# Kernel tuning notes

Measured on AMD Instinct MI355X. Metric: run time of the kernel, lower is better.

## Reference

```python
import jax, jax.numpy as jnp
import numpy as np

DIM = 512
HEADS = 8
DIM_HEAD = 64
SCALE = DIM_HEAD ** -0.5


def setup_inputs() -> dict:
    key = jax.random.key(0)
    k1, k2, k3, k4, k5 = jax.random.split(key, 5)
    inner = HEADS * DIM_HEAD
    x = jax.random.normal(k1, (16, DIM, 32, 32), dtype=jnp.float32)
    W_proj = jax.random.normal(k2, (DIM, inner * 3), dtype=jnp.float32) * (DIM ** -0.5)
    b_proj = jax.random.normal(k3, (inner * 3,), dtype=jnp.float32) * 0.01
    W_out = jax.random.normal(k4, (inner, DIM), dtype=jnp.float32) * (inner ** -0.5)
    b_out = jax.random.normal(k5, (DIM,), dtype=jnp.float32) * 0.01
    return {"x": x, "W_proj": W_proj, "b_proj": b_proj, "W_out": W_out, "b_out": b_out}


def reference(x, W_proj, b_proj, W_out, b_out):
    b, c, hh, ww = x.shape
    s = hh * ww
    xs = x.reshape(b, c, s).transpose(0, 2, 1)  # b s c
    qkv = xs @ W_proj + b_proj                  # b s (heads * 3*dim_head)
    qkv = qkv.reshape(b, s, HEADS, 3 * DIM_HEAD)
    q, k, v = jnp.split(qkv, 3, axis=-1)        # each: b s h d
    w = jnp.einsum('bshd,bthd->bsth', q, k) * SCALE
    w = jax.nn.softmax(w, axis=2)
    res = jnp.einsum('bsth,bthd->bshd', w, v).reshape(b, s, HEADS * DIM_HEAD)
    out = res @ W_out + b_out + xs              # b s c (residual)
    return out.transpose(0, 2, 1).reshape(b, c, hh, ww)
```

## Files before the change

kernel.cpp:

```cpp
#include <hip/hip_runtime.h>
#include <hip/hip_bf16.h>

#define BATCH 16
#define CDIM  512
#define SEQ   1024
#define HEADS 8
#define DHEAD 64
#define N3    1536
#define QSCALE 0.18033688011112042f

typedef unsigned short ushort_t;
typedef __attribute__((ext_vector_type(8))) short short8;
typedef __attribute__((ext_vector_type(4))) float f32x4;

__device__ __forceinline__ unsigned f2bf(float f) {
    unsigned u = __float_as_uint(f);
    u += 0x7fffu + ((u >> 16) & 1u);
    return u >> 16;
}
__device__ __forceinline__ float fast_exp2(float x) {
    float r;
    asm("v_exp_f32 %0, %1" : "=v"(r) : "v"(x));
    return r;
}
__device__ __forceinline__ unsigned pack_bf16_trunc(float lo, float hi) {
    return __builtin_amdgcn_perm(__float_as_uint(hi), __float_as_uint(lo), 0x07060302u);
}
__device__ __forceinline__ void async16(const void* g, void* l) {
    __builtin_amdgcn_global_load_lds(
        (const __attribute__((address_space(1))) unsigned int*)g,
        (__attribute__((address_space(3))) unsigned int*)l, 16, 0, 0);
}
__device__ __forceinline__ void barrier_raw() {
    __builtin_amdgcn_sched_barrier(0);
    __builtin_amdgcn_s_barrier();
    __builtin_amdgcn_sched_barrier(0);
}
#define WAIT_VMCNT(n) asm volatile("s_waitcnt vmcnt(" #n ")" ::: "memory")


__global__ __launch_bounds__(256) void blockify_kernel(
    const float* __restrict__ in, ushort_t* __restrict__ out, int C)
{
    __shared__ float t[64][65];
    const int k0 = blockIdx.y * 64, c0 = blockIdx.x * 64;
    const float* inb = in + (size_t)blockIdx.z * 512 * C;
    const int tid = threadIdx.x;
#pragma unroll
    for (int i = 0; i < 16; ++i) {
        int idx = tid + i * 256;
        int r = idx >> 6, c = idx & 63;
        t[r][c] = inb[(size_t)(k0 + r) * C + c0 + c];
    }
    __syncthreads();
    const size_t mbase = (size_t)blockIdx.z * C + c0;
    const int ml = tid & 63;
#pragma unroll
    for (int i = 0; i < 2; ++i) {
        int oct = (tid >> 6) + i * 4;
        size_t m = mbase + ml;
        int mt = (int)(m >> 7), mr = (int)(m & 127);
        int m16 = mr >> 4, col = mr & 15;
        int k = k0 + oct * 8;
        int it = k >> 5, q = (k >> 3) & 3;
        uint4 pk;
        pk.x = f2bf(t[oct * 8 + 0][ml]) | (f2bf(t[oct * 8 + 1][ml]) << 16);
        pk.y = f2bf(t[oct * 8 + 2][ml]) | (f2bf(t[oct * 8 + 3][ml]) << 16);
        pk.z = f2bf(t[oct * 8 + 4][ml]) | (f2bf(t[oct * 8 + 5][ml]) << 16);
        pk.w = f2bf(t[oct * 8 + 6][ml]) | (f2bf(t[oct * 8 + 7][ml]) << 16);
        size_t off = ((size_t)(mt * 16 + it) * 8 + m16) * 512 + (q * 16 + col) * 8;
        *(uint4*)&out[off] = pk;
    }
}

__global__ __launch_bounds__(256) void qkv_gemm_kernel(
    const ushort_t* __restrict__ xtb, const ushort_t* __restrict__ WpTb,
    const float* __restrict__ bp,
    ushort_t* __restrict__ q_buf, ushort_t* __restrict__ kb,
    ushort_t* __restrict__ vb)
{
    __shared__ alignas(16) ushort_t Asub[2][8 * 512];
    __shared__ alignas(16) ushort_t Bsub[2][8 * 512];

    const int tid = threadIdx.x, w = tid >> 6, lane = tid & 63;
    const int quad = lane >> 4, col = lane & 15;
    const int wm = w >> 1, wn = w & 1;

    const int lin = blockIdx.x + 12 * blockIdx.y;
    const int xcd = lin & 7;
    const int rr  = lin >> 3;
    const int n0  = (rr % 12) * 128;
    const int m0  = ((rr / 12) * 8 + xcd) * 128;

    f32x4 acc[4][4];
#pragma unroll
    for (int i = 0; i < 4; ++i)
#pragma unroll
        for (int j = 0; j < 4; ++j) acc[i][j] = (f32x4){0.f, 0.f, 0.f, 0.f};

    const ushort_t* Ab = xtb  + (size_t)(m0 >> 7) * 65536 + (w * 2) * 512 + lane * 8;
    const ushort_t* Bb = WpTb + (size_t)(n0 >> 7) * 65536 + (w * 2) * 512 + lane * 8;

#define QKV_STAGE(buf, t)                                         \
    do {                                                          \
        async16(Ab + (t) * 4096,       &Asub[buf][(w * 2 + 0) * 512]); \
        async16(Ab + (t) * 4096 + 512, &Asub[buf][(w * 2 + 1) * 512]); \
        async16(Bb + (t) * 4096,       &Bsub[buf][(w * 2 + 0) * 512]); \
        async16(Bb + (t) * 4096 + 512, &Bsub[buf][(w * 2 + 1) * 512]); \
    } while (0)

    QKV_STAGE(0, 0);
    QKV_STAGE(1, 1);
    for (int it = 0; it < 16; ++it) {
        const int cur = it & 1;
        if (it < 15) { WAIT_VMCNT(4); } else { WAIT_VMCNT(0); }
        barrier_raw();

        short8 af[4], bfr[4];
#pragma unroll
        for (int i = 0; i < 4; ++i) af[i]  = *(const short8*)&Asub[cur][(wm * 4 + i) * 512 + lane * 8];
#pragma unroll
        for (int j = 0; j < 4; ++j) bfr[j] = *(const short8*)&Bsub[cur][(wn * 4 + j) * 512 + lane * 8];
#pragma unroll
        for (int i = 0; i < 4; ++i)
#pragma unroll
            for (int j = 0; j < 4; ++j)
                acc[i][j] = __builtin_amdgcn_mfma_f32_16x16x32_bf16(af[i], bfr[j], acc[i][j], 0, 0, 0);

        if (it < 14) {
            barrier_raw();
            QKV_STAGE(cur, it + 2);
        }
    }
#undef QKV_STAGE

    const int b = m0 >> 10, s0 = m0 & 1023;
    const size_t b8 = (size_t)b * HEADS;
#pragma unroll
    for (int j = 0; j < 4; ++j) {
        int nb = n0 + wn * 64 + j * 16;
        int h = nb / 192, rem = nb % 192;
        int type = rem >> 6, dbase = rem & 63;
        float bias = bp[nb + col];
        size_t bh = b8 + h;
        int d = dbase + col;
#pragma unroll
        for (int i = 0; i < 4; ++i) {
            int sb = s0 + wm * 64 + i * 16 + quad * 4;
            f32x4 v = acc[i][j];
            if (type == 2) {
                unsigned lo = f2bf(v[0] + bias) | (f2bf(v[1] + bias) << 16);
                unsigned hi = f2bf(v[2] + bias) | (f2bf(v[3] + bias) << 16);
                uint2 pk; pk.x = lo; pk.y = hi;
                int itv = sb >> 6, sub = (d >> 4) * 2 + ((sb >> 5) & 1);
                size_t off = ((bh * 16 + itv) * 8 + sub) * 512
                           + (((sb >> 3) & 3) * 16 + (d & 15)) * 8 + (sb & 7);
                *(uint2*)&vb[off] = pk;
            } else if (type == 1) {
#pragma unroll
                for (int r = 0; r < 4; ++r) {
                    int t = sb + r;
                    int itk = t >> 6, sub = ((t >> 4) & 3) * 2 + (d >> 5);
                    size_t off = ((bh * 16 + itk) * 8 + sub) * 512
                               + (((d >> 3) & 3) * 16 + (t & 15)) * 8 + (d & 7);
                    kb[off] = (ushort_t)f2bf(v[r] + bias);
                }
            } else {
#pragma unroll
                for (int r = 0; r < 4; ++r)
                    q_buf[(bh * SEQ + sb + r) * DHEAD + d] =
                        (ushort_t)f2bf((v[r] + bias) * QSCALE);
            }
        }
    }
}

__global__ __launch_bounds__(128) void attn_kernel(
    const ushort_t* __restrict__ q_buf, const ushort_t* __restrict__ kb,
    const ushort_t* __restrict__ vb, ushort_t* __restrict__ resb)
{
    __shared__ alignas(16) ushort_t Kf[2][8 * 512];
    __shared__ alignas(16) ushort_t Vf[2][8 * 512];
    __shared__ alignas(16) ushort_t Pf[2 * 1024];

    const int tid  = threadIdx.x;
    const int w    = tid >> 6;
    const int lane = tid & 63;
    const int quad = lane >> 4;
    const int col  = lane & 15;

    const int bhid = blockIdx.x;
    const int b = bhid >> 3, h = bhid & 7;
    const int q0 = blockIdx.y * 128;
    const size_t bh = (size_t)b * HEADS + h;

    const ushort_t* qp = q_buf + ((bh * SEQ) + q0 + w * 64 + col) * DHEAD + quad * 8;
    short8 qf0[4], qf1[4];
#pragma unroll
    for (int g = 0; g < 4; ++g) {
        qf0[g] = *(const short8*)(qp + g * 16 * DHEAD);
        qf1[g] = *(const short8*)(qp + g * 16 * DHEAD + 32);
    }

    short8 ones;
#pragma unroll
    for (int i = 0; i < 8; ++i) ones[i] = (short)0x3F80;

    f32x4 O[4][4];
#pragma unroll
    for (int g = 0; g < 4; ++g)
#pragma unroll
        for (int i = 0; i < 4; ++i) O[g][i] = (f32x4){0.f, 0.f, 0.f, 0.f};
    f32x4 L[4];
#pragma unroll
    for (int g = 0; g < 4; ++g) L[g] = (f32x4){0.f, 0.f, 0.f, 0.f};

    const ushort_t* kaB = kb + (size_t)bh * 65536 + (w * 4) * 512 + lane * 8;
    const ushort_t* vaB = vb + (size_t)bh * 65536 + (w * 4) * 512 + lane * 8;

    const int poff_base = col * 8 + (quad & 1) * 4;
    const int qh = quad >> 1;
    ushort_t* pg = &Pf[w * 1024];

#define ATTN_STAGE(buf, t)                                          \
    do {                                                            \
        const ushort_t* ka_ = kaB + (size_t)(t) * 4096;             \
        const ushort_t* va_ = vaB + (size_t)(t) * 4096;             \
        async16(ka_,        &Kf[buf][(w * 4 + 0) * 512]);           \
        async16(ka_ + 512,  &Kf[buf][(w * 4 + 1) * 512]);           \
        async16(ka_ + 1024, &Kf[buf][(w * 4 + 2) * 512]);           \
        async16(ka_ + 1536, &Kf[buf][(w * 4 + 3) * 512]);           \
        async16(va_,        &Vf[buf][(w * 4 + 0) * 512]);           \
        async16(va_ + 512,  &Vf[buf][(w * 4 + 1) * 512]);           \
        async16(va_ + 1024, &Vf[buf][(w * 4 + 2) * 512]);           \
        async16(va_ + 1536, &Vf[buf][(w * 4 + 3) * 512]);           \
    } while (0)

    ATTN_STAGE(0, 0);
    ATTN_STAGE(1, 1);

    for (int it = 0; it < 16; ++it) {
        const int cur = it & 1;
        const ushort_t* kc = Kf[cur];
        const ushort_t* vc = Vf[cur];
        if (it < 15) { WAIT_VMCNT(8); } else { WAIT_VMCNT(0); }
        barrier_raw();

        short8 kf[8];
#pragma unroll
        for (int t16 = 0; t16 < 4; ++t16) {
            kf[2 * t16 + 0] = *(const short8*)&kc[(t16 * 2 + 0) * 512 + lane * 8];
            kf[2 * t16 + 1] = *(const short8*)&kc[(t16 * 2 + 1) * 512 + lane * 8];
        }

        short8 pf[4][2];
#pragma unroll
        for (int g = 0; g < 4; ++g) {
            f32x4 S[4];
            __builtin_amdgcn_s_setprio(1);
#pragma unroll
            for (int t16 = 0; t16 < 4; ++t16) {
                f32x4 a = (f32x4){0.f, 0.f, 0.f, 0.f};
                a = __builtin_amdgcn_mfma_f32_16x16x32_bf16(kf[2 * t16 + 0], qf0[g], a, 0, 0, 0);
                a = __builtin_amdgcn_mfma_f32_16x16x32_bf16(kf[2 * t16 + 1], qf1[g], a, 0, 0, 0);
                S[t16] = a;
            }
            __builtin_amdgcn_s_setprio(0);
#pragma unroll
            for (int t16 = 0; t16 < 4; ++t16) {
                uint2 pk;
                pk.x = pack_bf16_trunc(fast_exp2(S[t16][0]), fast_exp2(S[t16][1]));
                pk.y = pack_bf16_trunc(fast_exp2(S[t16][2]), fast_exp2(S[t16][3]));
                int off = (t16 >> 1) * 512 + (((t16 * 2) + qh) & 3) * 128 + poff_base;
                *(uint2*)&pg[off] = pk;
            }
            pf[g][0] = *(const short8*)&pg[lane * 8];
            pf[g][1] = *(const short8*)&pg[512 + lane * 8];
        }

#pragma unroll
        for (int d16 = 0; d16 < 4; ++d16) {
            const short8 v0 = *(const short8*)&vc[(d16 * 2 + 0) * 512 + lane * 8];
            const short8 v1 = *(const short8*)&vc[(d16 * 2 + 1) * 512 + lane * 8];
            __builtin_amdgcn_s_setprio(1);
#pragma unroll
            for (int g = 0; g < 4; ++g) {
                O[g][d16] = __builtin_amdgcn_mfma_f32_16x16x32_bf16(pf[g][0], v0, O[g][d16], 0, 0, 0);
                O[g][d16] = __builtin_amdgcn_mfma_f32_16x16x32_bf16(pf[g][1], v1, O[g][d16], 0, 0, 0);
            }
            __builtin_amdgcn_s_setprio(0);
        }
#pragma unroll
        for (int g = 0; g < 4; ++g) {
            L[g] = __builtin_amdgcn_mfma_f32_16x16x32_bf16(pf[g][0], ones, L[g], 0, 0, 0);
            L[g] = __builtin_amdgcn_mfma_f32_16x16x32_bf16(pf[g][1], ones, L[g], 0, 0, 0);
        }

        if (it < 14) {
            barrier_raw();
            ATTN_STAGE(cur, it + 2);
        }
    }
#undef ATTN_STAGE

    const int mt = b * 8 + (q0 >> 7);
#pragma unroll
    for (int g = 0; g < 4; ++g) {
        const int m16 = w * 4 + g;
#pragma unroll
        for (int r = 0; r < 4; ++r) {
            float inv = 1.f / L[g][r];
            const int mcol = quad * 4 + r;
#pragma unroll
            for (int d16 = 0; d16 < 4; ++d16) {
                int itk = h * 2 + (d16 >> 1);
                int kq = (d16 & 1) * 2 + (col >> 3);
                size_t off = ((size_t)(mt * 16 + itk) * 8 + m16) * 512
                           + (kq * 16 + mcol) * 8 + (col & 7);
                resb[off] = (ushort_t)f2bf(O[g][d16][r] * inv);
            }
        }
    }
}

__global__ __launch_bounds__(256) void out_gemm_kernel(
    const ushort_t* __restrict__ resb, const ushort_t* __restrict__ WoTb,
    const float* __restrict__ bo, const float* __restrict__ x,
    float* __restrict__ out)
{
    __shared__ alignas(16) ushort_t Asub[2][8 * 512];
    __shared__ alignas(16) ushort_t Bsub[2][8 * 512];

    const int tid = threadIdx.x, w = tid >> 6, lane = tid & 63;
    const int quad = lane >> 4, col = lane & 15;
    const int wm = w >> 1, wn = w & 1;

    const int lin = blockIdx.x + 4 * blockIdx.y;
    const int xcd = lin & 7;
    const int rr  = lin >> 3;
    const int n0  = (rr & 3) * 128;
    const int m0  = ((rr >> 2) * 8 + xcd) * 128;

    f32x4 acc[4][4];
#pragma unroll
    for (int i = 0; i < 4; ++i)
#pragma unroll
        for (int j = 0; j < 4; ++j) acc[i][j] = (f32x4){0.f, 0.f, 0.f, 0.f};

    const ushort_t* Ab = resb + (size_t)(m0 >> 7) * 65536 + (w * 2) * 512 + lane * 8;
    const ushort_t* Bb = WoTb + (size_t)(n0 >> 7) * 65536 + (w * 2) * 512 + lane * 8;

#define OUT_STAGE(buf, t)                                         \
    do {                                                          \
        async16(Ab + (t) * 4096,       &Asub[buf][(w * 2 + 0) * 512]); \
        async16(Ab + (t) * 4096 + 512, &Asub[buf][(w * 2 + 1) * 512]); \
        async16(Bb + (t) * 4096,       &Bsub[buf][(w * 2 + 0) * 512]); \
        async16(Bb + (t) * 4096 + 512, &Bsub[buf][(w * 2 + 1) * 512]); \
    } while (0)

    OUT_STAGE(0, 0);
    OUT_STAGE(1, 1);
    for (int it = 0; it < 16; ++it) {
        const int cur = it & 1;
        if (it < 15) { WAIT_VMCNT(4); } else { WAIT_VMCNT(0); }
        barrier_raw();

        short8 af[4], bfr[4];
#pragma unroll
        for (int i = 0; i < 4; ++i) af[i]  = *(const short8*)&Asub[cur][(wm * 4 + i) * 512 + lane * 8];
#pragma unroll
        for (int j = 0; j < 4; ++j) bfr[j] = *(const short8*)&Bsub[cur][(wn * 4 + j) * 512 + lane * 8];
#pragma unroll
        for (int i = 0; i < 4; ++i)
#pragma unroll
            for (int j = 0; j < 4; ++j)
                acc[i][j] = __builtin_amdgcn_mfma_f32_16x16x32_bf16(af[i], bfr[j], acc[i][j], 0, 0, 0);

        if (it < 14) {
            barrier_raw();
            OUT_STAGE(cur, it + 2);
        }
    }
#undef OUT_STAGE

    const int b = m0 >> 10, s0 = m0 & 1023;
#pragma unroll
    for (int j = 0; j < 4; ++j) {
        int n = n0 + wn * 64 + j * 16 + col;
        float bias = bo[n];
#pragma unroll
        for (int i = 0; i < 4; ++i) {
            int sb = s0 + wm * 64 + i * 16 + quad * 4;
            size_t o = ((size_t)b * CDIM + n) * SEQ + sb;
            float4 xr = *(const float4*)&x[o];
            f32x4 v = acc[i][j];
            float4 ov;
            ov.x = v[0] + bias + xr.x;
            ov.y = v[1] + bias + xr.y;
            ov.z = v[2] + bias + xr.z;
            ov.w = v[3] + bias + xr.w;
            *(float4*)&out[o] = ov;
        }
    }
}

extern "C" void kernel_launch(void* const* d_in, const int* in_sizes, int n_in,
                              void* d_out, int out_size, void* d_ws, size_t ws_size,
                              hipStream_t stream) {
    const float* x  = (const float*)d_in[0];
    const float* Wp = (const float*)d_in[1];
    const float* bp = (const float*)d_in[2];
    const float* Wo = (const float*)d_in[3];
    const float* bo = (const float*)d_in[4];
    float* out = (float*)d_out;

    ushort_t* xtb   = (ushort_t*)d_ws;
    ushort_t* WpTb  = xtb   + (size_t)8388608;
    ushort_t* WoTb  = WpTb  + (size_t)786432;
    ushort_t* q_buf = WoTb  + (size_t)262144;
    ushort_t* kb    = q_buf + (size_t)8388608;
    ushort_t* vb    = kb    + (size_t)8388608;
    ushort_t* resb  = vb    + (size_t)8388608;

    blockify_kernel<<<dim3(16, 8, 16), 256, 0, stream>>>(x,  xtb,  1024);
    blockify_kernel<<<dim3(24, 8, 1),  256, 0, stream>>>(Wp, WpTb, 1536);
    blockify_kernel<<<dim3(8, 8, 1),   256, 0, stream>>>(Wo, WoTb, 512);
    qkv_gemm_kernel<<<dim3(12, 128), 256, 0, stream>>>(xtb, WpTb, bp, q_buf, kb, vb);
    attn_kernel<<<dim3(128, 8), 128, 0, stream>>>(q_buf, kb, vb, resb);
    out_gemm_kernel<<<dim3(4, 128), 256, 0, stream>>>(resb, WoTb, bo, x, out);
}
```

Before: 194.0 us.

## Keep softmax probabilities in registers by permuting V layout; simplify prefetch pipeline

Rewrites the V buffer layout in the projection epilogue so the S accumulator fragments from the QK MFMA map directly onto the A operand of the PV MFMA. This removes the per-wave LDS round trip for P (the stores, the loads and the Pf shared buffer). The async K/V prefetch also changes from two stages issued after compute to one stage issued right after a __syncthreads at the top of each iteration. That replaces the explicit vmcnt waits, which may expose more load latency in exchange for simpler synchronisation.

Measured after the change: 196.0 us. Within noise of the previous version (+1.1%).

```diff
diff --git a/kernel.cpp b/kernel.cpp
--- a/kernel.cpp
+++ b/kernel.cpp
@@ -154,7 +154,8 @@
                 uint2 pk; pk.x = lo; pk.y = hi;
                 int itv = sb >> 6, sub = (d >> 4) * 2 + ((sb >> 5) & 1);
                 size_t off = ((bh * 16 + itv) * 8 + sub) * 512
-                           + (((sb >> 3) & 3) * 16 + (d & 15)) * 8 + (sb & 7);
+                           + (((sb >> 2) & 3) * 16 + (d & 15)) * 8
+                           + ((sb >> 4) & 1) * 4;
                 *(uint2*)&vb[off] = pk;
             } else if (type == 1) {
 #pragma unroll
@@ -181,7 +182,6 @@
 {
     __shared__ alignas(16) ushort_t Kf[2][8 * 512];
     __shared__ alignas(16) ushort_t Vf[2][8 * 512];
-    __shared__ alignas(16) ushort_t Pf[2 * 1024];
 
     const int tid  = threadIdx.x;
     const int w    = tid >> 6;
@@ -218,33 +218,28 @@
     const ushort_t* kaB = kb + (size_t)bh * 65536 + (w * 4) * 512 + lane * 8;
     const ushort_t* vaB = vb + (size_t)bh * 65536 + (w * 4) * 512 + lane * 8;
 
-    const int poff_base = col * 8 + (quad & 1) * 4;
-    const int qh = quad >> 1;
-    ushort_t* pg = &Pf[w * 1024];
-
-#define ATTN_STAGE(buf, t)                                          \
-    do {                                                            \
-        const ushort_t* ka_ = kaB + (size_t)(t) * 4096;             \
-        const ushort_t* va_ = vaB + (size_t)(t) * 4096;             \
-        async16(ka_,        &Kf[buf][(w * 4 + 0) * 512]);           \
-        async16(ka_ + 512,  &Kf[buf][(w * 4 + 1) * 512]);           \
-        async16(ka_ + 1024, &Kf[buf][(w * 4 + 2) * 512]);           \
-        async16(ka_ + 1536, &Kf[buf][(w * 4 + 3) * 512]);           \
-        async16(va_,        &Vf[buf][(w * 4 + 0) * 512]);           \
-        async16(va_ + 512,  &Vf[buf][(w * 4 + 1) * 512]);           \
-        async16(va_ + 1024, &Vf[buf][(w * 4 + 2) * 512]);           \
-        async16(va_ + 1536, &Vf[buf][(w * 4 + 3) * 512]);           \
+#define ATTN_STAGE(buf)                                            \
+    do {                                                           \
+        async16(kaB,        &Kf[buf][(w * 4 + 0) * 512]);          \
+        async16(kaB + 512,  &Kf[buf][(w * 4 + 1) * 512]);          \
+        async16(kaB + 1024, &Kf[buf][(w * 4 + 2) * 512]);          \
+        async16(kaB + 1536, &Kf[buf][(w * 4 + 3) * 512]);          \
+        async16(vaB,        &Vf[buf][(w * 4 + 0) * 512]);          \
+        async16(vaB + 512,  &Vf[buf][(w * 4 + 1) * 512]);          \
+        async16(vaB + 1024, &Vf[buf][(w * 4 + 2) * 512]);          \
+        async16(vaB + 1536, &Vf[buf][(w * 4 + 3) * 512]);          \
+        kaB += 4096;                                               \
+        vaB += 4096;                                               \
     } while (0)
 
-    ATTN_STAGE(0, 0);
-    ATTN_STAGE(1, 1);
+    ATTN_STAGE(0);
 
     for (int it = 0; it < 16; ++it) {
         const int cur = it & 1;
         const ushort_t* kc = Kf[cur];
         const ushort_t* vc = Vf[cur];
-        if (it < 15) { WAIT_VMCNT(8); } else { WAIT_VMCNT(0); }
-        barrier_raw();
+        __syncthreads();
+        if (it < 15) ATTN_STAGE(cur ^ 1);
 
         short8 kf[8];
 #pragma unroll
@@ -266,16 +261,17 @@
                 S[t16] = a;
             }
             __builtin_amdgcn_s_setprio(0);
-#pragma unroll
-            for (int t16 = 0; t16 < 4; ++t16) {
-                uint2 pk;
-                pk.x = pack_bf16_trunc(fast_exp2(S[t16][0]), fast_exp2(S[t16][1]));
-                pk.y = pack_bf16_trunc(fast_exp2(S[t16][2]), fast_exp2(S[t16][3]));
-                int off = (t16 >> 1) * 512 + (((t16 * 2) + qh) & 3) * 128 + poff_base;
-                *(uint2*)&pg[off] = pk;
-            }
-            pf[g][0] = *(const short8*)&pg[lane * 8];
-            pf[g][1] = *(const short8*)&pg[512 + lane * 8];
+            union { uint4 u; short8 s; } p0, p1;
+            p0.u.x = pack_bf16_trunc(fast_exp2(S[0][0]), fast_exp2(S[0][1]));
+            p0.u.y = pack_bf16_trunc(fast_exp2(S[0][2]), fast_exp2(S[0][3]));
+            p0.u.z = pack_bf16_trunc(fast_exp2(S[1][0]), fast_exp2(S[1][1]));
+            p0.u.w = pack_bf16_trunc(fast_exp2(S[1][2]), fast_exp2(S[1][3]));
+            p1.u.x = pack_bf16_trunc(fast_exp2(S[2][0]), fast_exp2(S[2][1]));
+            p1.u.y = pack_bf16_trunc(fast_exp2(S[2][2]), fast_exp2(S[2][3]));
+            p1.u.z = pack_bf16_trunc(fast_exp2(S[3][0]), fast_exp2(S[3][1]));
+            p1.u.w = pack_bf16_trunc(fast_exp2(S[3][2]), fast_exp2(S[3][3]));
+            pf[g][0] = p0.s;
+            pf[g][1] = p1.s;
         }
 
 #pragma unroll
@@ -294,11 +290,6 @@
         for (int g = 0; g < 4; ++g) {
             L[g] = __builtin_amdgcn_mfma_f32_16x16x32_bf16(pf[g][0], ones, L[g], 0, 0, 0);
             L[g] = __builtin_amdgcn_mfma_f32_16x16x32_bf16(pf[g][1], ones, L[g], 0, 0, 0);
-        }
-
-        if (it < 14) {
-            barrier_raw();
-            ATTN_STAGE(cur, it + 2);
         }
     }
 #undef ATTN_STAGE
```
